# Performance work log

Hardware: AMD Instinct MI355X
Metric: run time of the kernel (lower is better)

## Reference

```python
import jax, jax.numpy as jnp
import numpy as np

N = 100000


def gcn_conv(x, edge_index, W, b):
    """PyG GCNConv: h = D^-1/2 (A+I) D^-1/2 (x W) + b, scatter-add at targets."""
    n = x.shape[0]
    src, dst = edge_index[0], edge_index[1]
    # add self-loops
    loop = jnp.arange(n, dtype=src.dtype)
    src = jnp.concatenate([src, loop])
    dst = jnp.concatenate([dst, loop])
    # degree of target nodes (with self-loops), symmetric normalization
    deg = jax.ops.segment_sum(jnp.ones_like(dst, dtype=x.dtype), dst, num_segments=n)
    dinv = jnp.where(deg > 0, jax.lax.rsqrt(deg), 0.0)
    norm = dinv[src] * dinv[dst]                     # [E+N]
    h = x @ W                                        # [N, out] transform first (small dim)
    msg = h[src] * norm[:, None]                     # gather + scale
    out = jax.ops.segment_sum(msg, dst, num_segments=n)  # scatter-add
    return out + b


def setup_inputs() -> dict:
    key = jax.random.key(0)
    k1, k2, k3, k4, k5 = jax.random.split(key, 5)
    x = jax.random.normal(k1, (N, 128), dtype=jnp.float32)
    edge_index = jax.random.randint(k2, (2, 1600000), 0, N, dtype=jnp.int64)
    # glorot-ish init for linear weights, zero bias (PyG default)
    W1 = jax.random.normal(k3, (128, 64), dtype=jnp.float32) * (1.0 / np.sqrt(128))
    b1 = jnp.zeros((64,), dtype=jnp.float32)
    W2 = jax.random.normal(k4, (64, 32), dtype=jnp.float32) * (1.0 / np.sqrt(64))
    b2 = jnp.zeros((32,), dtype=jnp.float32)
    return {"x": x, "edge_index": edge_index, "W1": W1, "b1": b1, "W2": W2, "b2": b2}


def reference(x, edge_index, W1, b1, W2, b2):
    h = gcn_conv(x, edge_index, W1, b1)
    h = jax.nn.relu(h)
    # dropout is identity in eval mode (training=False)
    out = gcn_conv(h, edge_index, W2, b2)
    return out
```

## Files before the change

### kernel.cpp

```cpp
#include <hip/hip_runtime.h>

typedef unsigned int   u32;
typedef unsigned short u16;
typedef __attribute__((ext_vector_type(8))) short bf16x8;
typedef __attribute__((ext_vector_type(4))) float f32x4;

__device__ __forceinline__ u16 f2b(float f) {
    u32 u = __float_as_uint(f);
    u += 0x7FFFu + ((u >> 16) & 1u);
    return (u16)(u >> 16);
}
__device__ __forceinline__ float b2f_lo(u32 v) { return __uint_as_float(v << 16); }
__device__ __forceinline__ float b2f_hi(u32 v) { return __uint_as_float(v & 0xFFFF0000u); }
__device__ __forceinline__ u32 pack2(float a, float b) {
    return (u32)f2b(a) | ((u32)f2b(b) << 16);
}

#define BSHIFT 8
#define BIN_CHUNK 4096
#define CAP_MAX 8192


__global__ __launch_bounds__(256) void k_bin(const int* __restrict__ src,
                                             const int* __restrict__ dst,
                                             int* __restrict__ bcnt,
                                             u32* __restrict__ binned,
                                             int E, int NB, int CAP) {
    __shared__ int lh[512], ls[512], gb[512], sh[256];
    __shared__ u32 stage[BIN_CHUNK];
    __shared__ u16 sbuck[BIN_CHUNK];
    int tid = threadIdx.x;
    int base = blockIdx.x * BIN_CHUNK;
    int cnt = E - base;
    if (cnt > BIN_CHUNK) cnt = BIN_CHUNK;

    for (int i = tid; i < 512; i += 256) lh[i] = 0;
    __syncthreads();

    int bk[16], r[16];
    u32 key[16];
#pragma unroll
    for (int t = 0; t < 16; t++) {
        int i = base + t * 256 + tid;
        bk[t] = -1;
        if (i < E) {
            int dv = dst[i];
            bk[t] = dv >> BSHIFT;
            key[t] = ((u32)(dv & 255) << 24) | (u32)src[i];
            r[t] = atomicAdd(&lh[bk[t]], 1);
        }
    }
    __syncthreads();
    {
        int a0 = lh[2 * tid], a1 = lh[2 * tid + 1];
        int sum2 = a0 + a1;
        sh[tid] = sum2;
        __syncthreads();
        for (int dd = 1; dd < 256; dd <<= 1) {
            int x = tid >= dd ? sh[tid - dd] : 0;
            __syncthreads();
            sh[tid] += x;
            __syncthreads();
        }
        int excl = sh[tid] - sum2;
        ls[2 * tid] = excl;
        ls[2 * tid + 1] = excl + a0;
    }
    for (int b = tid; b < NB; b += 256) {
        int c = lh[b];
        gb[b] = c ? atomicAdd(&bcnt[b], c) : 0;
    }
    __syncthreads();
#pragma unroll
    for (int t = 0; t < 16; t++) {
        if (bk[t] >= 0) {
            int slot = ls[bk[t]] + r[t];
            stage[slot] = key[t];
            sbuck[slot] = (u16)bk[t];
        }
    }
    __syncthreads();
    for (int j = tid; j < cnt; j += 256) {
        u32 e = stage[j];
        int b = sbuck[j];
        int p = gb[b] + (j - ls[b]);
        if (p < CAP) binned[(size_t)b * CAP + p] = e;
    }
}

__global__ __launch_bounds__(256) void k_csr(const u32* __restrict__ binned,
                                             const int* __restrict__ bcnt,
                                             float* __restrict__ dinv,
                                             int2* __restrict__ offse,
                                             int* __restrict__ esrc,
                                             int n, int CAP) {
    __shared__ int lcnt[256], lcur[256], sh[256];
    __shared__ u32 stagec[CAP_MAX];
    int tid = threadIdx.x;
    int b = blockIdx.x;
    size_t base = (size_t)b * CAP;
    int ecnt = bcnt[b];
    if (ecnt > CAP) ecnt = CAP;
    lcnt[tid] = 0;
    __syncthreads();
    for (int j = tid; j < ecnt; j += 256) {
        u32 e = binned[base + j];
        stagec[j] = e;
        atomicAdd(&lcnt[e >> 24], 1);
    }
    __syncthreads();
    int v = lcnt[tid];
    sh[tid] = v;
    __syncthreads();
    for (int d = 1; d < 256; d <<= 1) {
        int x = tid >= d ? sh[tid - d] : 0;
        __syncthreads();
        sh[tid] += x;
        __syncthreads();
    }
    int excl = sh[tid] - v;
    int node = (b << BSHIFT) + tid;
    if (node < n) {
        offse[node] = make_int2((int)base + excl, (int)base + excl + v);
        dinv[node] = rsqrtf((float)(v + 1));
    }
    lcur[tid] = excl;
    __syncthreads();
    for (int j = tid; j < ecnt; j += 256) {
        u32 e = stagec[j];
        int p = atomicAdd(&lcur[e >> 24], 1);
        esrc[base + p] = (int)(e & 0xFFFFFFu);
    }
}


__global__ void k_prepW(const float* __restrict__ W1, bf16x8* __restrict__ Wpack) {
    int lane = threadIdx.x;
#pragma unroll
    for (int ct = 0; ct < 4; ct++) {
#pragma unroll
        for (int ks = 0; ks < 4; ks++) {
            bf16x8 h;
#pragma unroll
            for (int j = 0; j < 8; j++) {
                int k = ks * 32 + ((lane >> 4) << 3) + j;
                int col = ct * 16 + (lane & 15);
                h[j] = (short)f2b(W1[k * 64 + col]);
            }
            Wpack[(ct * 4 + ks) * 64 + lane] = h;
        }
    }
}


__global__ __launch_bounds__(256) void k_gemm1_mfma(const float* __restrict__ x,
                                                    const bf16x8* __restrict__ Wpack,
                                                    const float* __restrict__ dinv,
                                                    u16* __restrict__ h1b,
                                                    int n, int ntiles) {
    int gwave = (int)((blockIdx.x * blockDim.x + threadIdx.x) >> 6);
    int lane = threadIdx.x & 63;
    if (gwave >= ntiles) return;
    int rowBase = gwave * 16;

    bf16x8 bfr[16];
#pragma unroll
    for (int f = 0; f < 16; f++) bfr[f] = Wpack[f * 64 + lane];

    f32x4 acc[4];
#pragma unroll
    for (int ct = 0; ct < 4; ct++) acc[ct] = (f32x4){0.f, 0.f, 0.f, 0.f};

    int r0 = rowBase + (lane & 15);
    if (r0 >= n) r0 = n - 1;
    const float* xr = x + (size_t)r0 * 128 + ((lane >> 4) << 3);

#pragma unroll
    for (int ks = 0; ks < 4; ks++) {
        float4 p0 = *(const float4*)(xr + ks * 32);
        float4 p1 = *(const float4*)(xr + ks * 32 + 4);
        bf16x8 a;
        a[0] = (short)f2b(p0.x); a[1] = (short)f2b(p0.y);
        a[2] = (short)f2b(p0.z); a[3] = (short)f2b(p0.w);
        a[4] = (short)f2b(p1.x); a[5] = (short)f2b(p1.y);
        a[6] = (short)f2b(p1.z); a[7] = (short)f2b(p1.w);
#pragma unroll
        for (int ct = 0; ct < 4; ct++)
            acc[ct] = __builtin_amdgcn_mfma_f32_16x16x32_bf16(a, bfr[ct * 4 + ks], acc[ct], 0, 0, 0);
    }

    int rbase = rowBase + ((lane >> 4) << 2);
#pragma unroll
    for (int r = 0; r < 4; r++) {
        int row = rbase + r;
        float dv = (row < n) ? dinv[row] : 0.f;
#pragma unroll
        for (int ct = 0; ct < 4; ct++) {
            float o = acc[ct][r] * dv;
            float onb = __shfl_xor(o, 1);
            if (!(lane & 1) && row < n) {
                *(u32*)&h1b[(size_t)row * 64 + ct * 16 + (lane & 15)] = pack2(o, onb);
            }
        }
    }
}


__global__ __launch_bounds__(256) void k_agg1gemm2(const u16* __restrict__ h1b,
                                                   const int2* __restrict__ offse,
                                                   const int* __restrict__ esrc,
                                                   const float* __restrict__ dinv,
                                                   const float* __restrict__ b1,
                                                   const float* __restrict__ W2,
                                                   u16* __restrict__ h2b, int n) {
    __shared__ float aggL[4][64];
    int warp = threadIdx.x >> 6, lane = threadIdx.x & 63;
    int half = lane >> 5, c2 = lane & 31;
    float w2r[32];
#pragma unroll
    for (int kk = 0; kk < 32; kk++) w2r[kk] = W2[(half * 32 + kk) * 32 + c2];
    float2 bb = *(const float2*)&b1[2 * c2];
    int nwaves = (gridDim.x * blockDim.x) >> 6;
    for (int wid = (int)((blockIdx.x * blockDim.x + threadIdx.x) >> 6); wid < n;
         wid += nwaves) {
        int2 ov = offse[wid];
        int e1 = ov.y;
        float a0 = 0.f, a1 = 0.f, a2 = 0.f, a3 = 0.f;
        if (half == 0) {
            u32 v = *(const u32*)&h1b[(size_t)wid * 64 + 2 * c2];
            a0 += b2f_lo(v); a1 += b2f_hi(v);
        }
        int e = ov.x + half;
        for (; e + 2 < e1; e += 4) {
            int s0 = esrc[e], s1 = esrc[e + 2];
            u32 v0 = *(const u32*)&h1b[(size_t)s0 * 64 + 2 * c2];
            u32 v1 = *(const u32*)&h1b[(size_t)s1 * 64 + 2 * c2];
            a0 += b2f_lo(v0); a1 += b2f_hi(v0);
            a2 += b2f_lo(v1); a3 += b2f_hi(v1);
        }
        if (e < e1) {
            int s = esrc[e];
            u32 v = *(const u32*)&h1b[(size_t)s * 64 + 2 * c2];
            a0 += b2f_lo(v); a1 += b2f_hi(v);
        }
        a0 += a2; a1 += a3;
        a0 += __shfl_xor(a0, 32);
        a1 += __shfl_xor(a1, 32);
        float dv = dinv[wid];
        a0 = a0 * dv + bb.x; a1 = a1 * dv + bb.y;
        a0 = a0 > 0.f ? a0 : 0.f;
        a1 = a1 > 0.f ? a1 : 0.f;
        if (half == 0) *(float2*)&aggL[warp][2 * c2] = make_float2(a0, a1);
        asm volatile("s_waitcnt lgkmcnt(0)" ::: "memory");
        float acc = 0.f;
#pragma unroll
        for (int kk = 0; kk < 32; kk += 4) {
            float4 av = *(const float4*)&aggL[warp][half * 32 + kk];
            acc += av.x * w2r[kk] + av.y * w2r[kk + 1] + av.z * w2r[kk + 2] + av.w * w2r[kk + 3];
        }
        acc += __shfl_xor(acc, 32);
        if (half == 0) h2b[(size_t)wid * 32 + c2] = f2b(acc * dv);
    }
}


__global__ __launch_bounds__(256) void k_agg2(const u16* __restrict__ h2b,
                                              const int2* __restrict__ offse,
                                              const int* __restrict__ esrc,
                                              const float* __restrict__ dinv,
                                              const float* __restrict__ b2,
                                              float* __restrict__ out, int n) {
    int wid = (int)((blockIdx.x * blockDim.x + threadIdx.x) >> 6);
    int lane = threadIdx.x & 63;
    int g = lane >> 4, c2 = lane & 15;
    if (wid >= n) return;
    int2 ov = offse[wid];
    int e1 = ov.y;
    float a0 = 0.f, a1 = 0.f, a2 = 0.f, a3 = 0.f;
    int e = ov.x + g;
    for (; e + 4 < e1; e += 8) {
        int s0 = esrc[e], s1 = esrc[e + 4];
        u32 v0 = *(const u32*)&h2b[(size_t)s0 * 32 + 2 * c2];
        u32 v1 = *(const u32*)&h2b[(size_t)s1 * 32 + 2 * c2];
        a0 += b2f_lo(v0); a1 += b2f_hi(v0);
        a2 += b2f_lo(v1); a3 += b2f_hi(v1);
    }
    if (e < e1) {
        int s = esrc[e];
        u32 v = *(const u32*)&h2b[(size_t)s * 32 + 2 * c2];
        a0 += b2f_lo(v); a1 += b2f_hi(v);
    }
    a0 += a2; a1 += a3;
    a0 += __shfl_xor(a0, 16); a0 += __shfl_xor(a0, 32);
    a1 += __shfl_xor(a1, 16); a1 += __shfl_xor(a1, 32);
    if (g == 0) {
        u32 v = *(const u32*)&h2b[(size_t)wid * 32 + 2 * c2];
        a0 += b2f_lo(v); a1 += b2f_hi(v);
        float dv = dinv[wid];
        float2 o = make_float2(a0 * dv + b2[2 * c2], a1 * dv + b2[2 * c2 + 1]);
        *(float2*)&out[(size_t)wid * 32 + 2 * c2] = o;
    }
}


extern "C" void kernel_launch(void* const* d_in, const int* in_sizes, int n_in,
                              void* d_out, int out_size, void* d_ws, size_t ws_size,
                              hipStream_t stream) {
    const float* x  = (const float*)d_in[0];
    const int*   ei = (const int*)d_in[1];
    const float* W1 = (const float*)d_in[2];
    const float* b1 = (const float*)d_in[3];
    const float* W2 = (const float*)d_in[4];
    const float* b2 = (const float*)d_in[5];
    float* out = (float*)d_out;

    const int n = in_sizes[0] / 128;
    const int E = in_sizes[1] / 2;
    const int* src = ei;
    const int* dst = ei + E;
    const int NB = (n + 255) >> BSHIFT;
    int avg = (E + NB - 1) / NB;
    int CAP = avg + avg / 8 + 512;
    if (CAP > CAP_MAX) CAP = CAP_MAX;

    char* ws = (char*)d_ws;
    size_t woff = 0;
    auto carve = [&](size_t bytes) {
        void* p = ws + woff;
        woff += (bytes + 255) & ~(size_t)255;
        return p;
    };
    int*    bcnt   = (int*)carve((size_t)NB * sizeof(int));
    u32*    binned = (u32*)carve((size_t)NB * CAP * sizeof(u32));
    int2*   offse  = (int2*)carve((size_t)n * sizeof(int2));
    float*  dinv   = (float*)carve((size_t)n * sizeof(float));
    int*    esrc   = (int*)carve((size_t)NB * CAP * sizeof(int));
    bf16x8* Wpack  = (bf16x8*)carve(16 * 64 * sizeof(bf16x8));
    u16*    h1b    = (u16*)carve((size_t)n * 64 * sizeof(u16));
    u16*    h2b    = (u16*)carve((size_t)n * 32 * sizeof(u16));

    const int B = 256;
    const int ntiles16 = (n + 15) / 16;

    hipMemsetAsync(bcnt, 0, (size_t)NB * sizeof(int), stream);
    k_prepW<<<1, 64, 0, stream>>>(W1, Wpack);

    k_bin<<<(E + BIN_CHUNK - 1) / BIN_CHUNK, B, 0, stream>>>(src, dst, bcnt, binned, E, NB, CAP);
    k_csr<<<NB, B, 0, stream>>>(binned, bcnt, dinv, offse, esrc, n, CAP);

    k_gemm1_mfma<<<(ntiles16 + 3) / 4, B, 0, stream>>>(x, Wpack, dinv, h1b, n, ntiles16);

    k_agg1gemm2<<<2048, B, 0, stream>>>(h1b, offse, esrc, dinv, b1, W2, h2b, n);

    k_agg2<<<(n + 3) / 4, B, 0, stream>>>(h2b, offse, esrc, dinv, b2, out, n);
}
```

Baseline: 164.8 us.

## Fuse CSR build with first GEMM and merge init kernels

```diff
diff --git a/kernel.cpp b/kernel.cpp
--- a/kernel.cpp
+++ b/kernel.cpp
@@ -17,8 +17,32 @@
 }
 
 #define BSHIFT 8
-#define BIN_CHUNK 4096
-#define CAP_MAX 8192
+#define BIN_CHUNK 2048
+#define CAP_MAX 6144
+
+
+__global__ void k_init(const float* __restrict__ W1, bf16x8* __restrict__ Wpack,
+                       int* __restrict__ bcnt, int NB) {
+    int tid = threadIdx.x;
+    for (int i = tid; i < NB; i += 256) bcnt[i] = 0;
+    if (tid < 64) {
+        int lane = tid;
+#pragma unroll
+        for (int ct = 0; ct < 4; ct++) {
+#pragma unroll
+            for (int ks = 0; ks < 4; ks++) {
+                bf16x8 h;
+#pragma unroll
+                for (int j = 0; j < 8; j++) {
+                    int k = ks * 32 + ((lane >> 4) << 3) + j;
+                    int col = ct * 16 + (lane & 15);
+                    h[j] = (short)f2b(W1[k * 64 + col]);
+                }
+                Wpack[(ct * 4 + ks) * 64 + lane] = h;
+            }
+        }
+    }
+}
 
 
 __global__ __launch_bounds__(256) void k_bin(const int* __restrict__ src,
@@ -37,10 +61,11 @@
     for (int i = tid; i < 512; i += 256) lh[i] = 0;
     __syncthreads();
 
-    int bk[16], r[16];
-    u32 key[16];
-#pragma unroll
-    for (int t = 0; t < 16; t++) {
+    const int T = BIN_CHUNK / 256;
+    int bk[T], r[T];
+    u32 key[T];
+#pragma unroll
+    for (int t = 0; t < T; t++) {
         int i = base + t * 256 + tid;
         bk[t] = -1;
         if (i < E) {
@@ -72,7 +97,7 @@
     }
     __syncthreads();
 #pragma unroll
-    for (int t = 0; t < 16; t++) {
+    for (int t = 0; t < T; t++) {
         if (bk[t] >= 0) {
             int slot = ls[bk[t]] + r[t];
             stage[slot] = key[t];
@@ -88,17 +113,23 @@
     }
 }
 
-__global__ __launch_bounds__(256) void k_csr(const u32* __restrict__ binned,
-                                             const int* __restrict__ bcnt,
-                                             float* __restrict__ dinv,
-                                             int2* __restrict__ offse,
-                                             int* __restrict__ esrc,
-                                             int n, int CAP) {
+
+__global__ __launch_bounds__(256) void k_csr_gemm1(const u32* __restrict__ binned,
+                                                   const int* __restrict__ bcnt,
+                                                   const bf16x8* __restrict__ Wpack,
+                                                   const float* __restrict__ x,
+                                                   float* __restrict__ dinv,
+                                                   int2* __restrict__ offse,
+                                                   int* __restrict__ esrc,
+                                                   u16* __restrict__ h1b,
+                                                   int n, int CAP) {
+    __shared__ u32 stagec[CAP_MAX];
     __shared__ int lcnt[256], lcur[256], sh[256];
-    __shared__ u32 stagec[CAP_MAX];
+    __shared__ float dinv_sh[256];
     int tid = threadIdx.x;
     int b = blockIdx.x;
     size_t base = (size_t)b * CAP;
+    int nodeBase = b << BSHIFT;
     int ecnt = bcnt[b];
     if (ecnt > CAP) ecnt = CAP;
     lcnt[tid] = 0;
@@ -113,16 +144,18 @@
     sh[tid] = v;
     __syncthreads();
     for (int d = 1; d < 256; d <<= 1) {
-        int x = tid >= d ? sh[tid - d] : 0;
+        int xx = tid >= d ? sh[tid - d] : 0;
         __syncthreads();
-        sh[tid] += x;
+        sh[tid] += xx;
         __syncthreads();
     }
     int excl = sh[tid] - v;
-    int node = (b << BSHIFT) + tid;
+    int node = nodeBase + tid;
+    float dvt = rsqrtf((float)(v + 1));
+    dinv_sh[tid] = dvt;
     if (node < n) {
         offse[node] = make_int2((int)base + excl, (int)base + excl + v);
-        dinv[node] = rsqrtf((float)(v + 1));
+        dinv[node] = dvt;
     }
     lcur[tid] = excl;
     __syncthreads();
@@ -131,75 +164,48 @@
         int p = atomicAdd(&lcur[e >> 24], 1);
         esrc[base + p] = (int)(e & 0xFFFFFFu);
     }
-}
-
-
-__global__ void k_prepW(const float* __restrict__ W1, bf16x8* __restrict__ Wpack) {
-    int lane = threadIdx.x;
-#pragma unroll
-    for (int ct = 0; ct < 4; ct++) {
+
+    int wv = tid >> 6, lane = tid & 63;
+    bf16x8 bfr[16];
+#pragma unroll
+    for (int f = 0; f < 16; f++) bfr[f] = Wpack[f * 64 + lane];
+
+    for (int t = wv; t < 16; t += 4) {
+        int rowBase = nodeBase + t * 16;
+        if (rowBase >= n) break;
+        f32x4 acc[4];
+#pragma unroll
+        for (int ct = 0; ct < 4; ct++) acc[ct] = (f32x4){0.f, 0.f, 0.f, 0.f};
+
+        int r0 = rowBase + (lane & 15);
+        if (r0 >= n) r0 = n - 1;
+        const float* xr = x + (size_t)r0 * 128 + ((lane >> 4) << 3);
 #pragma unroll
         for (int ks = 0; ks < 4; ks++) {
-            bf16x8 h;
-#pragma unroll
-            for (int j = 0; j < 8; j++) {
-                int k = ks * 32 + ((lane >> 4) << 3) + j;
-                int col = ct * 16 + (lane & 15);
-                h[j] = (short)f2b(W1[k * 64 + col]);
-            }
-            Wpack[(ct * 4 + ks) * 64 + lane] = h;
-        }
-    }
-}
-
-
-__global__ __launch_bounds__(256) void k_gemm1_mfma(const float* __restrict__ x,
-                                                    const bf16x8* __restrict__ Wpack,
-                                                    const float* __restrict__ dinv,
-                                                    u16* __restrict__ h1b,
-                                                    int n, int ntiles) {
-    int gwave = (int)((blockIdx.x * blockDim.x + threadIdx.x) >> 6);
-    int lane = threadIdx.x & 63;
-    if (gwave >= ntiles) return;
-    int rowBase = gwave * 16;
-
-    bf16x8 bfr[16];
-#pragma unroll
-    for (int f = 0; f < 16; f++) bfr[f] = Wpack[f * 64 + lane];
-
-    f32x4 acc[4];
-#pragma unroll
-    for (int ct = 0; ct < 4; ct++) acc[ct] = (f32x4){0.f, 0.f, 0.f, 0.f};
-
-    int r0 = rowBase + (lane & 15);
-    if (r0 >= n) r0 = n - 1;
-    const float* xr = x + (size_t)r0 * 128 + ((lane >> 4) << 3);
-
-#pragma unroll
-    for (int ks = 0; ks < 4; ks++) {
-        float4 p0 = *(const float4*)(xr + ks * 32);
-        float4 p1 = *(const float4*)(xr + ks * 32 + 4);
-        bf16x8 a;
-        a[0] = (short)f2b(p0.x); a[1] = (short)f2b(p0.y);
-        a[2] = (short)f2b(p0.z); a[3] = (short)f2b(p0.w);
-        a[4] = (short)f2b(p1.x); a[5] = (short)f2b(p1.y);
-        a[6] = (short)f2b(p1.z); a[7] = (short)f2b(p1.w);
-#pragma unroll
-        for (int ct = 0; ct < 4; ct++)
-            acc[ct] = __builtin_amdgcn_mfma_f32_16x16x32_bf16(a, bfr[ct * 4 + ks], acc[ct], 0, 0, 0);
-    }
-
-    int rbase = rowBase + ((lane >> 4) << 2);
-#pragma unroll
-    for (int r = 0; r < 4; r++) {
-        int row = rbase + r;
-        float dv = (row < n) ? dinv[row] : 0.f;
-#pragma unroll
-        for (int ct = 0; ct < 4; ct++) {
-            float o = acc[ct][r] * dv;
-            float onb = __shfl_xor(o, 1);
-            if (!(lane & 1) && row < n) {
-                *(u32*)&h1b[(size_t)row * 64 + ct * 16 + (lane & 15)] = pack2(o, onb);
+            float4 p0 = *(const float4*)(xr + ks * 32);
+            float4 p1 = *(const float4*)(xr + ks * 32 + 4);
+            bf16x8 a;
+            a[0] = (short)f2b(p0.x); a[1] = (short)f2b(p0.y);
+            a[2] = (short)f2b(p0.z); a[3] = (short)f2b(p0.w);
+            a[4] = (short)f2b(p1.x); a[5] = (short)f2b(p1.y);
+            a[6] = (short)f2b(p1.z); a[7] = (short)f2b(p1.w);
+#pragma unroll
+            for (int ct = 0; ct < 4; ct++)
+                acc[ct] = __builtin_amdgcn_mfma_f32_16x16x32_bf16(a, bfr[ct * 4 + ks], acc[ct], 0, 0, 0);
+        }
+        int lrb = t * 16 + ((lane >> 4) << 2);
+#pragma unroll
+        for (int r = 0; r < 4; r++) {
+            int lrow = lrb + r;
+            int row = nodeBase + lrow;
+            float dv = dinv_sh[lrow];
+#pragma unroll
+            for (int ct = 0; ct < 4; ct++) {
+                float o = acc[ct][r] * dv;
+                float onb = __shfl_xor(o, 1);
+                if (!(lane & 1) && row < n) {
+                    *(u32*)&h1b[(size_t)row * 64 + ct * 16 + (lane & 15)] = pack2(o, onb);
+                }
             }
         }
     }
@@ -340,15 +346,12 @@
     u16*    h2b    = (u16*)carve((size_t)n * 32 * sizeof(u16));
 
     const int B = 256;
-    const int ntiles16 = (n + 15) / 16;
-
-    hipMemsetAsync(bcnt, 0, (size_t)NB * sizeof(int), stream);
-    k_prepW<<<1, 64, 0, stream>>>(W1, Wpack);
+
+    k_init<<<1, B, 0, stream>>>(W1, Wpack, bcnt, NB);
 
     k_bin<<<(E + BIN_CHUNK - 1) / BIN_CHUNK, B, 0, stream>>>(src, dst, bcnt, binned, E, NB, CAP);
-    k_csr<<<NB, B, 0, stream>>>(binned, bcnt, dinv, offse, esrc, n, CAP);
-
-    k_gemm1_mfma<<<(ntiles16 + 3) / 4, B, 0, stream>>>(x, Wpack, dinv, h1b, n, ntiles16);
+
+    k_csr_gemm1<<<NB, B, 0, stream>>>(binned, bcnt, Wpack, x, dinv, offse, esrc, h1b, n, CAP);
 
     k_agg1gemm2<<<2048, B, 0, stream>>>(h1b, offse, esrc, dinv, b1, W2, h2b, n);
 
```

After: 164.7 us, median of 2. Within noise of the previous version (-0.0%).
